# Optimization experiments

Hardware: AMD Instinct MI355X
Metric: run time of the kernel (lower is better)

Reference implementation:

```python
import jax, jax.numpy as jnp
import numpy as np

GRID = 32
N_NODES = GRID * GRID          # 1024
PATCH = 1
C_IN = 3
NODE_F = C_IN * PATCH * PATCH  # 3
HID = 256
N_CLASSES = 10


def _build_norm_adj():
    # 5-point grid stencil + self loops, symmetrically normalized: D^-1/2 A D^-1/2
    adj = np.zeros((N_NODES, N_NODES), dtype=np.float32)
    idx = np.arange(N_NODES)
    i, j = idx // GRID, idx % GRID
    adj[idx, idx] = 1.0
    for di, dj in [(-1, 0), (1, 0), (0, -1), (0, 1)]:
        ni, nj = i + di, j + dj
        ok = (ni >= 0) & (ni < GRID) & (nj >= 0) & (nj < GRID)
        adj[idx[ok], (ni * GRID + nj)[ok]] = 1.0
    deg = adj.sum(axis=1)
    dis = np.where(deg > 0, deg ** -0.5, 0.0).astype(np.float32)
    return jnp.asarray(dis[:, None] * adj * dis[None, :])


def _image_to_graph(x):
    # [B,C,H,W] -> [B, grid, patch, grid, patch] blocks -> [B, N, C*patch^2]
    B = x.shape[0]
    x = x.reshape(B, C_IN, GRID, PATCH, GRID, PATCH)
    x = jnp.transpose(x, (0, 2, 4, 1, 3, 5))
    return x.reshape(B, N_NODES, NODE_F)


def setup_inputs() -> dict:
    key = jax.random.key(0)
    ks = jax.random.split(key, 10)
    s = 0.05
    return {
        "x": jax.random.normal(ks[0], (256, 3, 32, 32), dtype=jnp.float32),
        "W1": jax.random.normal(ks[1], (HID, NODE_F), dtype=jnp.float32) * s,
        "b1": jnp.zeros((HID,), dtype=jnp.float32),
        "W2": jax.random.normal(ks[2], (HID, HID), dtype=jnp.float32) * s,
        "b2": jnp.zeros((HID,), dtype=jnp.float32),
        "W3": jax.random.normal(ks[3], (HID // 2, HID), dtype=jnp.float32) * s,
        "b3": jnp.zeros((HID // 2,), dtype=jnp.float32),
        "Wc": jax.random.normal(ks[4], (N_CLASSES, N_NODES * (HID // 2)), dtype=jnp.float32) * s,
        "bc": jnp.zeros((N_CLASSES,), dtype=jnp.float32),
        "adj": _build_norm_adj(),
    }


def _gc(h, W, b, adj):
    # Linear, then fixed-adjacency aggregation, then ReLU
    h = jnp.einsum('bnf,hf->bnh', h, W) + b
    h = jnp.einsum('mn,bnh->bmh', adj, h)
    return jax.nn.relu(h)


def reference(x, W1, b1, W2, b2, W3, b3, Wc, bc, adj):
    h = _image_to_graph(x)                 # [B, N, 3]
    h = _gc(h, W1, b1, adj)                # [B, N, 256]
    h = _gc(h, W2, b2, adj)                # [B, N, 256]
    h = _gc(h, W3, b3, adj)                # [B, N, 128]
    h = h.reshape(h.shape[0], -1)          # [B, N*128]
    return h @ Wc.T + bc                   # [B, 10]
```

## Files before the change

### kernel.cpp

```cpp
#include <hip/hip_runtime.h>
#include <stdint.h>

#define N_NODES 1024
#define NCLS 10
#define KDIM 131072

typedef unsigned short u16;
typedef __bf16 bf16x8 __attribute__((ext_vector_type(8)));
typedef float f32x4 __attribute__((ext_vector_type(4)));

__device__ __forceinline__ float b2f_lo(uint32_t u) {
  union { float f; uint32_t u; } v; v.u = u << 16; return v.f;
}
__device__ __forceinline__ float b2f_hi(uint32_t u) {
  union { float f; uint32_t u; } v; v.u = u & 0xFFFF0000u; return v.f;
}
__device__ __forceinline__ u16 f2b(float f) {
  union { float f; uint32_t u; } v; v.f = f;
  uint32_t r = v.u + 0x7FFF + ((v.u >> 16) & 1);
  return (u16)(r >> 16);
}
__device__ __forceinline__ uint32_t pkbf(float a, float b) {
#if __has_builtin(__builtin_amdgcn_cvt_pk_bf16_f32)
  typedef __bf16 bf2 __attribute__((ext_vector_type(2)));
  bf2 r = __builtin_amdgcn_cvt_pk_bf16_f32(a, b);
  union { bf2 v; uint32_t u; } c; c.v = r; return c.u;
#else
  union { float f; uint32_t u; } va, vb; va.f = a; vb.f = b;
  uint32_t ra = (va.u + 0x7FFF + ((va.u >> 16) & 1)) >> 16;
  uint32_t rb = (vb.u + 0x7FFF + ((vb.u >> 16) & 1)) & 0xFFFF0000u;
  return ra | rb;
#endif
}

__device__ __forceinline__ void async_copy16(const u16* g, u16* l) {
  __builtin_amdgcn_global_load_lds(
      (const __attribute__((address_space(1))) void*)g,
      (__attribute__((address_space(3))) void*)l, 16, 0, 0);
}

__device__ __forceinline__ void agg8(uint4 v, float c, float2* acc) {
  const uint32_t* u = (const uint32_t*)&v;
#pragma unroll
  for (int e = 0; e < 4; e++) {
    acc[e].x += c * b2f_lo(u[e]);
    acc[e].y += c * b2f_hi(u[e]);
  }
}

__global__ __launch_bounds__(256) void cvt_w_kernel(const float* __restrict__ w,
                                                    u16* __restrict__ o, int n) {
  int i = blockIdx.x * 256 + threadIdx.x;
  if (i < n) o[i] = f2b(w[i]);
}

__global__ __launch_bounds__(256) void prep_wc_kernel(const float* __restrict__ wc,
                                                      u16* __restrict__ o) {
  int i = blockIdx.x * 256 + threadIdx.x;
  int row = i >> 17;
  int col = i & (KDIM - 1);
  o[i] = (row < NCLS) ? f2b(wc[row * KDIM + col]) : (u16)0;
}

__global__ __launch_bounds__(256) void prep_tab_kernel(const float* __restrict__ adj,
                                                       int* __restrict__ nbi,
                                                       float* __restrict__ nbc,
                                                       float* __restrict__ r) {
  int m = blockIdx.x * 256 + threadIdx.x;
  if (m >= N_NODES) return;
  int i = m >> 5, j = m & 31;
  const float* arow = adj + (size_t)m * N_NODES;
  int n[5]; float c[5];
  n[0] = m;                      c[0] = arow[m];
  n[1] = (i > 0)  ? m - 32 : m;  c[1] = (i > 0)  ? arow[m - 32] : 0.f;
  n[2] = (i < 31) ? m + 32 : m;  c[2] = (i < 31) ? arow[m + 32] : 0.f;
  n[3] = (j > 0)  ? m - 1  : m;  c[3] = (j > 0)  ? arow[m - 1]  : 0.f;
  n[4] = (j < 31) ? m + 1  : m;  c[4] = (j < 31) ? arow[m + 1]  : 0.f;
  float s = 0.f;
#pragma unroll
  for (int t = 0; t < 5; t++) { nbi[m * 5 + t] = n[t]; nbc[m * 5 + t] = c[t]; s += c[t]; }
  r[m] = s;
}

__global__ __launch_bounds__(256) void outinit_kernel(const float* __restrict__ bc,
                                                      float* __restrict__ out) {
  int idx = blockIdx.x * 256 + threadIdx.x;
  if (idx < 256 * NCLS) out[idx] = bc[idx % NCLS];
}

__global__ __launch_bounds__(256) void l1agg_kernel(
    const float* __restrict__ x,
    const float* __restrict__ W1,
    const float* __restrict__ b1,
    const int* __restrict__ nbi, const float* __restrict__ nbc,
    const float* __restrict__ r,
    u16* __restrict__ g)
{
  __shared__ u16 h1s[128 * 256];
  __shared__ float gxs[128][4];
  __shared__ float W1s[768];
  __shared__ float b1s[256];
  int p0 = blockIdx.x * 64;
  int b = p0 >> 10;
  int m0 = p0 & 1023;
  int e0 = m0 - 32;
  int tid = threadIdx.x;

  b1s[tid] = b1[tid];
  for (int i = tid; i < 768; i += 256) W1s[i] = W1[i];

  if (tid < 128) {
    int n = e0 + tid;
    float g0 = 0.f, g1 = 0.f, g2 = 0.f, rn = 0.f;
    if (n >= 0 && n < N_NODES) {
      const float* xb = x + (size_t)b * 3072;
#pragma unroll
      for (int t = 0; t < 5; t++) {
        int nb = nbi[n * 5 + t]; float cf = nbc[n * 5 + t];
        g0 += cf * xb[nb];
        g1 += cf * xb[1024 + nb];
        g2 += cf * xb[2048 + nb];
      }
      rn = r[n];
    }
    gxs[tid][0] = g0; gxs[tid][1] = g1; gxs[tid][2] = g2; gxs[tid][3] = rn;
  }
  __syncthreads();

  int ch8 = (tid & 31) * 8;
  float w[8][3], bb[8];
#pragma unroll
  for (int c = 0; c < 8; c++) {
    w[c][0] = W1s[(ch8 + c) * 3];
    w[c][1] = W1s[(ch8 + c) * 3 + 1];
    w[c][2] = W1s[(ch8 + c) * 3 + 2];
    bb[c] = b1s[ch8 + c];
  }

#pragma unroll
  for (int it = 0; it < 16; it++) {
    int node = (tid >> 5) + it * 8;
    float g0 = gxs[node][0], g1 = gxs[node][1], g2 = gxs[node][2], rn = gxs[node][3];
    uint32_t pk[4];
#pragma unroll
    for (int c = 0; c < 8; c += 2) {
      float z0 = fmaxf(g0 * w[c][0] + g1 * w[c][1] + g2 * w[c][2] + rn * bb[c], 0.f);
      float z1 = fmaxf(g0 * w[c+1][0] + g1 * w[c+1][1] + g2 * w[c+1][2] + rn * bb[c+1], 0.f);
      pk[c >> 1] = pkbf(z0, z1);
    }
    *(uint4*)&h1s[node * 256 + ch8] = *(uint4*)pk;
  }
  __syncthreads();

#pragma unroll
  for (int it = 0; it < 8; it++) {
    int node = (tid >> 5) + it * 8;
    int m = m0 + node;
    float2 acc[4] = {};
#pragma unroll
    for (int t = 0; t < 5; t++) {
      int nb = nbi[m * 5 + t]; float cf = nbc[m * 5 + t];
      agg8(*(const uint4*)&h1s[(nb - e0) * 256 + ch8], cf, acc);
    }
    uint4 o;
    o.x = pkbf(acc[0].x, acc[0].y); o.y = pkbf(acc[1].x, acc[1].y);
    o.z = pkbf(acc[2].x, acc[2].y); o.w = pkbf(acc[3].x, acc[3].y);
    *(uint4*)&g[(size_t)(p0 + node) * 256 + ch8] = o;
  }
}

__global__ __launch_bounds__(256, 2) void mm_kernel(
    const u16* __restrict__ A, const u16* __restrict__ W,
    const float* __restrict__ bias, const float* __restrict__ r,
    u16* __restrict__ C, int N)
{
  const int K = 256;
  __shared__ u16 As[2][128 * 64];
  __shared__ u16 Bs[2][128 * 64];
  int n0 = blockIdx.x * 128;
  int m0 = blockIdx.y * 128;
  int tid = threadIdx.x;
  int w = tid >> 6, l = tid & 63;
  int wm = w >> 1, wn = w & 1;

  int r8 = l >> 3, oct = l & 7;
  int so = (oct ^ r8) << 3;
  const u16* ga0 = A + (size_t)(m0 + w * 32 + r8) * K + so;
  const u16* gb0 = W + (size_t)(n0 + w * 32 + r8) * K + so;

#define MM_ISSUE(kq, buf) \
  _Pragma("unroll") for (int q = 0; q < 4; q++) { \
    async_copy16(ga0 + (size_t)q * 8 * K + (kq) * 64, &As[buf][(w * 32 + q * 8) * 64]); \
    async_copy16(gb0 + (size_t)q * 8 * K + (kq) * 64, &Bs[buf][(w * 32 + q * 8) * 64]); \
  }

  MM_ISSUE(0, 0);

  f32x4 acc[4][4] = {};
  int lrow = l & 15, lq = l >> 4;
  int s = lrow & 7;

#pragma unroll
  for (int kq = 0; kq < 4; kq++) {
    int buf = kq & 1;
    __syncthreads();
    if (kq < 3) MM_ISSUE(kq + 1, buf ^ 1);
    const u16* pa = &As[buf][(wm * 64 + lrow) * 64];
    const u16* pb = &Bs[buf][(wn * 64 + lrow) * 64];
#pragma unroll
    for (int kh = 0; kh < 2; kh++) {
      int po = (((kh << 2) | lq) ^ s) << 3;
      bf16x8 af[4], bf[4];
#pragma unroll
      for (int t = 0; t < 4; t++) {
        af[t] = *(const bf16x8*)(pa + t * 16 * 64 + po);
        bf[t] = *(const bf16x8*)(pb + t * 16 * 64 + po);
      }
#pragma unroll
      for (int mt = 0; mt < 4; mt++)
#pragma unroll
        for (int nt = 0; nt < 4; nt++)
          acc[mt][nt] = __builtin_amdgcn_mfma_f32_16x16x32_bf16(af[mt], bf[nt], acc[mt][nt], 0, 0, 0);
    }
  }
#undef MM_ISSUE

#pragma unroll
  for (int mt = 0; mt < 4; mt++)
#pragma unroll
    for (int nt = 0; nt < 4; nt++) {
      f32x4 v = acc[mt][nt];
      int col = n0 + wn * 64 + nt * 16 + lrow;
      float bs = bias[col];
#pragma unroll
      for (int i2 = 0; i2 < 4; i2++) {
        int row = m0 + wm * 64 + mt * 16 + lq * 4 + i2;
        float val = v[i2] + r[row & 1023] * bs;
        C[(size_t)row * N + col] = f2b(fmaxf(val, 0.f));
      }
    }
}

__global__ __launch_bounds__(256, 2) void mm3agg_kernel(
    const u16* __restrict__ H,
    const u16* __restrict__ W,
    const float* __restrict__ bias, const float* __restrict__ r,
    const int* __restrict__ nbi, const float* __restrict__ nbc,
    u16* __restrict__ C)
{
  const int K = 256, N = 128;
  const int AST = 72;
  __shared__ u16 As[2][128 * AST];
  __shared__ u16 Bs[2][128 * 64];
  int m0 = blockIdx.x * 128;
  int tid = threadIdx.x;
  int w = tid >> 6, l = tid & 63;
  int wm = w >> 1, wn = w & 1;

  int arow = tid >> 1;
  int acol = (tid & 1) * 32;
  int pg = m0 + arow;
  int node = pg & 1023;
  const u16* hb = H + ((size_t)(pg >> 10) << 10) * 256 + acol;
  const u16* nbp[5]; float cf[5];
#pragma unroll
  for (int j = 0; j < 5; j++) {
    nbp[j] = hb + (size_t)nbi[node * 5 + j] * 256;
    cf[j] = nbc[node * 5 + j];
  }

  int r8 = l >> 3, oct = l & 7;
  int so = (oct ^ r8) << 3;
  const u16* gb0 = W + (size_t)(w * 32 + r8) * K + so;

#define M3_ISSUEB(kq, buf) \
  _Pragma("unroll") for (int q = 0; q < 4; q++) \
    async_copy16(gb0 + (size_t)q * 8 * K + (kq) * 64, &Bs[buf][(w * 32 + q * 8) * 64]);

#define M3_LOADA(kq) \
  _Pragma("unroll") for (int j = 0; j < 5; j++) \
    _Pragma("unroll") for (int q = 0; q < 4; q++) \
      L[j][q] = *(const uint4*)(nbp[j] + (kq) * 64 + q * 8);

#define M3_AGGSTORE(buf) { \
  u16* dst = &As[buf][arow * AST + acol]; \
  _Pragma("unroll") for (int q = 0; q < 4; q++) { \
    float2 acc2[4] = {}; \
    _Pragma("unroll") for (int j = 0; j < 5; j++) agg8(L[j][q], cf[j], acc2); \
    uint4 o; \
    o.x = pkbf(acc2[0].x, acc2[0].y); o.y = pkbf(acc2[1].x, acc2[1].y); \
    o.z = pkbf(acc2[2].x, acc2[2].y); o.w = pkbf(acc2[3].x, acc2[3].y); \
    *(uint4*)(dst + q * 8) = o; \
  } }

  uint4 L[5][4];
  M3_ISSUEB(0, 0);
  M3_LOADA(0);
  M3_AGGSTORE(0);

  f32x4 acc[4][4] = {};
  int lrow = l & 15, lq = l >> 4;
  int s = lrow & 7;

#pragma unroll
  for (int kq = 0; kq < 4; kq++) {
    int buf = kq & 1;
    __syncthreads();
    if (kq < 3) {
      M3_ISSUEB(kq + 1, buf ^ 1);
      M3_LOADA(kq + 1);
    }
    const u16* pa = &As[buf][(wm * 64 + lrow) * AST];
    const u16* pb = &Bs[buf][(wn * 64 + lrow) * 64];
#pragma unroll
    for (int kh = 0; kh < 2; kh++) {
      int po = (((kh << 2) | lq) ^ s) << 3;
      bf16x8 af[4], bf[4];
#pragma unroll
      for (int t = 0; t < 4; t++) {
        af[t] = *(const bf16x8*)(pa + t * 16 * AST + kh * 32 + lq * 8);
        bf[t] = *(const bf16x8*)(pb + t * 16 * 64 + po);
      }
#pragma unroll
      for (int mt = 0; mt < 4; mt++)
#pragma unroll
        for (int nt = 0; nt < 4; nt++)
          acc[mt][nt] = __builtin_amdgcn_mfma_f32_16x16x32_bf16(af[mt], bf[nt], acc[mt][nt], 0, 0, 0);
    }
    if (kq < 3) M3_AGGSTORE(buf ^ 1);
  }
#undef M3_ISSUEB
#undef M3_LOADA
#undef M3_AGGSTORE

#pragma unroll
  for (int mt = 0; mt < 4; mt++)
#pragma unroll
    for (int nt = 0; nt < 4; nt++) {
      f32x4 v = acc[mt][nt];
      int col = wn * 64 + nt * 16 + lrow;
      float bs = bias[col];
#pragma unroll
      for (int i2 = 0; i2 < 4; i2++) {
        int row = m0 + wm * 64 + mt * 16 + lq * 4 + i2;
        float val = v[i2] + r[row & 1023] * bs;
        C[(size_t)row * N + col] = f2b(fmaxf(val, 0.f));
      }
    }
}

__global__ __launch_bounds__(256) void cls_kernel(
    const u16* __restrict__ h3,
    const u16* __restrict__ Wcb,
    float* __restrict__ out,
    int b0)
{
  int mt = blockIdx.x;
  int split = blockIdx.y;
  int w = threadIdx.x >> 6, l = threadIdx.x & 63;
  int lrow = l & 15, lq = l >> 4;
  f32x4 acc = {};
  int kbase = split * 4096 + w * 1024;
  const u16* pa = h3 + (size_t)(mt * 16 + lrow) * KDIM + kbase + lq * 8;
  const u16* pb = Wcb + (size_t)lrow * KDIM + kbase + lq * 8;
#pragma unroll 4
  for (int kk = 0; kk < 1024; kk += 32) {
    bf16x8 a = *(const bf16x8*)(pa + kk);
    bf16x8 b = *(const bf16x8*)(pb + kk);
    acc = __builtin_amdgcn_mfma_f32_16x16x32_bf16(a, b, acc, 0, 0, 0);
  }
  if (lrow < NCLS) {
#pragma unroll
    for (int i2 = 0; i2 < 4; i2++) {
      int b = b0 + mt * 16 + lq * 4 + i2;
      atomicAdd(&out[b * NCLS + lrow], acc[i2]);
    }
  }
}

extern "C" void kernel_launch(void* const* d_in, const int* in_sizes, int n_in,
                              void* d_out, int out_size, void* d_ws, size_t ws_size,
                              hipStream_t stream) {
  const float* x   = (const float*)d_in[0];
  const float* W1  = (const float*)d_in[1];
  const float* b1  = (const float*)d_in[2];
  const float* W2  = (const float*)d_in[3];
  const float* b2  = (const float*)d_in[4];
  const float* W3  = (const float*)d_in[5];
  const float* b3  = (const float*)d_in[6];
  const float* Wc  = (const float*)d_in[7];
  const float* bc  = (const float*)d_in[8];
  const float* adj = (const float*)d_in[9];
  float* out = (float*)d_out;
  const int B = 256;

  uint8_t* ws = (uint8_t*)d_ws;
  u16* W2b = (u16*)ws;  ws += (size_t)256 * 256 * 2;
  u16* W3b = (u16*)ws;  ws += (size_t)128 * 256 * 2;
  u16* Wcb = (u16*)ws;  ws += (size_t)16 * KDIM * 2;
  float* rr  = (float*)ws; ws += 1024 * 4;
  int*   nbi = (int*)ws;   ws += 1024 * 5 * 4;
  float* nbc = (float*)ws; ws += 1024 * 5 * 4;
  uintptr_t al = ((uintptr_t)ws + 255) & ~(uintptr_t)255;
  ws = (uint8_t*)al;
  size_t used = (size_t)(ws - (uint8_t*)d_ws);
  size_t avail = (ws_size > used) ? ws_size - used : 0;
  int chunk = 256;
  while (chunk > 32 && (size_t)chunk * 1024 * 256 * 2 * 2 > avail) chunk >>= 1;
  u16* bufA = (u16*)ws;
  u16* bufB = bufA + (size_t)chunk * 1024 * 256;

  cvt_w_kernel<<<256, 256, 0, stream>>>(W2, W2b, 256 * 256);
  cvt_w_kernel<<<128, 256, 0, stream>>>(W3, W3b, 128 * 256);
  prep_wc_kernel<<<(16 * KDIM) / 256, 256, 0, stream>>>(Wc, Wcb);
  prep_tab_kernel<<<4, 256, 0, stream>>>(adj, nbi, nbc, rr);
  outinit_kernel<<<(256 * NCLS + 255) / 256, 256, 0, stream>>>(bc, out);

  for (int b0 = 0; b0 < B; b0 += chunk) {
    const float* xb = x + (size_t)b0 * 3 * 1024;
    int M = chunk * 1024;
    l1agg_kernel<<<M / 64, 256, 0, stream>>>(xb, W1, b1, nbi, nbc, rr, bufB);
    {
      dim3 g(2, M / 128);
      mm_kernel<<<g, 256, 0, stream>>>(bufB, W2b, b2, rr, bufA, 256);
    }
    mm3agg_kernel<<<M / 128, 256, 0, stream>>>(bufA, W3b, b3, rr, nbi, nbc, bufB);
    dim3 gc(chunk / 16, 32);
    cls_kernel<<<gc, 256, 0, stream>>>(bufB, Wcb, out, b0);
  }
}
```

Before: 349.6 us.

## Halve GEMM K-tile to 32, raise occupancy, and use packed f32x2 math

Both GEMM kernels (mm_kernel and the fused aggregate+GEMM mm3agg_kernel) now stage 32-wide K slices instead of 64, with 8 pipeline steps instead of 4. This shrinks LDS use and register pressure, so launch bounds rise to 4 and 3 blocks per SM. The XOR swizzle on B tiles is dropped in favour of a plain 32-column layout, which may add LDS bank conflicts. Aggregation and layer-1 elementwise math are rewritten with f32x2 vectors to encourage packed FMA instructions. More barriers per tile are the trade-off.

```diff
diff --git a/kernel.cpp b/kernel.cpp
--- a/kernel.cpp
+++ b/kernel.cpp
@@ -8,6 +8,7 @@
 typedef unsigned short u16;
 typedef __bf16 bf16x8 __attribute__((ext_vector_type(8)));
 typedef float f32x4 __attribute__((ext_vector_type(4)));
+typedef float f32x2 __attribute__((ext_vector_type(2)));
 
 __device__ __forceinline__ float b2f_lo(uint32_t u) {
   union { float f; uint32_t u; } v; v.u = u << 16; return v.f;
@@ -32,6 +33,7 @@
   return ra | rb;
 #endif
 }
+__device__ __forceinline__ uint32_t pkbf2(f32x2 z) { return pkbf(z.x, z.y); }
 
 __device__ __forceinline__ void async_copy16(const u16* g, u16* l) {
   __builtin_amdgcn_global_load_lds(
@@ -39,12 +41,13 @@
       (__attribute__((address_space(3))) void*)l, 16, 0, 0);
 }
 
-__device__ __forceinline__ void agg8(uint4 v, float c, float2* acc) {
+__device__ __forceinline__ void agg8p(uint4 v, float c, f32x2* acc) {
   const uint32_t* u = (const uint32_t*)&v;
+  f32x2 cv = {c, c};
 #pragma unroll
   for (int e = 0; e < 4; e++) {
-    acc[e].x += c * b2f_lo(u[e]);
-    acc[e].y += c * b2f_hi(u[e]);
+    f32x2 p = {b2f_lo(u[e]), b2f_hi(u[e])};
+    acc[e] += p * cv;
   }
 }
 
@@ -128,25 +131,29 @@
   __syncthreads();
 
   int ch8 = (tid & 31) * 8;
-  float w[8][3], bb[8];
-#pragma unroll
-  for (int c = 0; c < 8; c++) {
-    w[c][0] = W1s[(ch8 + c) * 3];
-    w[c][1] = W1s[(ch8 + c) * 3 + 1];
-    w[c][2] = W1s[(ch8 + c) * 3 + 2];
-    bb[c] = b1s[ch8 + c];
+  f32x2 wp[3][4], bp[4];
+#pragma unroll
+  for (int p = 0; p < 4; p++) {
+    int c = ch8 + 2 * p;
+    wp[0][p] = (f32x2){W1s[c * 3],     W1s[(c + 1) * 3]};
+    wp[1][p] = (f32x2){W1s[c * 3 + 1], W1s[(c + 1) * 3 + 1]};
+    wp[2][p] = (f32x2){W1s[c * 3 + 2], W1s[(c + 1) * 3 + 2]};
+    bp[p]    = (f32x2){b1s[c],         b1s[c + 1]};
   }
 
 #pragma unroll
   for (int it = 0; it < 16; it++) {
     int node = (tid >> 5) + it * 8;
-    float g0 = gxs[node][0], g1 = gxs[node][1], g2 = gxs[node][2], rn = gxs[node][3];
+    f32x2 g0v = {gxs[node][0], gxs[node][0]};
+    f32x2 g1v = {gxs[node][1], gxs[node][1]};
+    f32x2 g2v = {gxs[node][2], gxs[node][2]};
+    f32x2 rnv = {gxs[node][3], gxs[node][3]};
     uint32_t pk[4];
 #pragma unroll
-    for (int c = 0; c < 8; c += 2) {
-      float z0 = fmaxf(g0 * w[c][0] + g1 * w[c][1] + g2 * w[c][2] + rn * bb[c], 0.f);
-      float z1 = fmaxf(g0 * w[c+1][0] + g1 * w[c+1][1] + g2 * w[c+1][2] + rn * bb[c+1], 0.f);
-      pk[c >> 1] = pkbf(z0, z1);
+    for (int p = 0; p < 4; p++) {
+      f32x2 z = g0v * wp[0][p] + g1v * wp[1][p] + g2v * wp[2][p] + rnv * bp[p];
+      z.x = fmaxf(z.x, 0.f); z.y = fmaxf(z.y, 0.f);
+      pk[p] = pkbf2(z);
     }
     *(uint4*)&h1s[node * 256 + ch8] = *(uint4*)pk;
   }
@@ -156,72 +163,67 @@
   for (int it = 0; it < 8; it++) {
     int node = (tid >> 5) + it * 8;
     int m = m0 + node;
-    float2 acc[4] = {};
+    f32x2 acc[4] = {};
 #pragma unroll
     for (int t = 0; t < 5; t++) {
       int nb = nbi[m * 5 + t]; float cf = nbc[m * 5 + t];
-      agg8(*(const uint4*)&h1s[(nb - e0) * 256 + ch8], cf, acc);
+      agg8p(*(const uint4*)&h1s[(nb - e0) * 256 + ch8], cf, acc);
     }
     uint4 o;
-    o.x = pkbf(acc[0].x, acc[0].y); o.y = pkbf(acc[1].x, acc[1].y);
-    o.z = pkbf(acc[2].x, acc[2].y); o.w = pkbf(acc[3].x, acc[3].y);
+    o.x = pkbf2(acc[0]); o.y = pkbf2(acc[1]);
+    o.z = pkbf2(acc[2]); o.w = pkbf2(acc[3]);
     *(uint4*)&g[(size_t)(p0 + node) * 256 + ch8] = o;
   }
 }
 
-__global__ __launch_bounds__(256, 2) void mm_kernel(
+__global__ __launch_bounds__(256, 4) void mm_kernel(
     const u16* __restrict__ A, const u16* __restrict__ W,
     const float* __restrict__ bias, const float* __restrict__ r,
     u16* __restrict__ C, int N)
 {
   const int K = 256;
-  __shared__ u16 As[2][128 * 64];
-  __shared__ u16 Bs[2][128 * 64];
+  __shared__ u16 As[2][128 * 32];
+  __shared__ u16 Bs[2][128 * 32];
   int n0 = blockIdx.x * 128;
   int m0 = blockIdx.y * 128;
   int tid = threadIdx.x;
   int w = tid >> 6, l = tid & 63;
   int wm = w >> 1, wn = w & 1;
 
-  int r8 = l >> 3, oct = l & 7;
-  int so = (oct ^ r8) << 3;
-  const u16* ga0 = A + (size_t)(m0 + w * 32 + r8) * K + so;
-  const u16* gb0 = W + (size_t)(n0 + w * 32 + r8) * K + so;
+  int srow = w * 16 + (l >> 2);
+  int skoff = (l & 3) * 8;
+  const u16* ga0 = A + (size_t)(m0 + srow) * K + skoff;
+  const u16* gb0 = W + (size_t)(n0 + srow) * K + skoff;
 
 #define MM_ISSUE(kq, buf) \
-  _Pragma("unroll") for (int q = 0; q < 4; q++) { \
-    async_copy16(ga0 + (size_t)q * 8 * K + (kq) * 64, &As[buf][(w * 32 + q * 8) * 64]); \
-    async_copy16(gb0 + (size_t)q * 8 * K + (kq) * 64, &Bs[buf][(w * 32 + q * 8) * 64]); \
+  _Pragma("unroll") for (int q = 0; q < 2; q++) { \
+    async_copy16(ga0 + (size_t)q * 64 * K + (kq) * 32, &As[buf][(q * 64 + w * 16) * 32]); \
+    async_copy16(gb0 + (size_t)q * 64 * K + (kq) * 32, &Bs[buf][(q * 64 + w * 16) * 32]); \
   }
 
   MM_ISSUE(0, 0);
 
   f32x4 acc[4][4] = {};
   int lrow = l & 15, lq = l >> 4;
-  int s = lrow & 7;
-
-#pragma unroll
-  for (int kq = 0; kq < 4; kq++) {
+
+#pragma unroll
+  for (int kq = 0; kq < 8; kq++) {
     int buf = kq & 1;
     __syncthreads();
-    if (kq < 3) MM_ISSUE(kq + 1, buf ^ 1);
-    const u16* pa = &As[buf][(wm * 64 + lrow) * 64];
-    const u16* pb = &Bs[buf][(wn * 64 + lrow) * 64];
-#pragma unroll
-    for (int kh = 0; kh < 2; kh++) {
-      int po = (((kh << 2) | lq) ^ s) << 3;
-      bf16x8 af[4], bf[4];
-#pragma unroll
-      for (int t = 0; t < 4; t++) {
-        af[t] = *(const bf16x8*)(pa + t * 16 * 64 + po);
-        bf[t] = *(const bf16x8*)(pb + t * 16 * 64 + po);
-      }
-#pragma unroll
-      for (int mt = 0; mt < 4; mt++)
-#pragma unroll
-        for (int nt = 0; nt < 4; nt++)
-          acc[mt][nt] = __builtin_amdgcn_mfma_f32_16x16x32_bf16(af[mt], bf[nt], acc[mt][nt], 0, 0, 0);
-    }
+    if (kq < 7) MM_ISSUE(kq + 1, buf ^ 1);
+    const u16* pa = &As[buf][(wm * 64 + lrow) * 32 + lq * 8];
+    const u16* pb = &Bs[buf][(wn * 64 + lrow) * 32 + lq * 8];
+    bf16x8 af[4], bf[4];
+#pragma unroll
+    for (int t = 0; t < 4; t++) {
+      af[t] = *(const bf16x8*)(pa + t * 16 * 32);
+      bf[t] = *(const bf16x8*)(pb + t * 16 * 32);
+    }
+#pragma unroll
+    for (int mt = 0; mt < 4; mt++)
+#pragma unroll
+      for (int nt = 0; nt < 4; nt++)
+        acc[mt][nt] = __builtin_amdgcn_mfma_f32_16x16x32_bf16(af[mt], bf[nt], acc[mt][nt], 0, 0, 0);
   }
 #undef MM_ISSUE
 
@@ -241,7 +243,7 @@
     }
 }
 
-__global__ __launch_bounds__(256, 2) void mm3agg_kernel(
+__global__ __launch_bounds__(256, 3) void mm3agg_kernel(
     const u16* __restrict__ H,
     const u16* __restrict__ W,
     const float* __restrict__ bias, const float* __restrict__ r,
@@ -249,16 +251,16 @@
     u16* __restrict__ C)
 {
   const int K = 256, N = 128;
-  const int AST = 72;
+  const int AST = 40;
   __shared__ u16 As[2][128 * AST];
-  __shared__ u16 Bs[2][128 * 64];
+  __shared__ u16 Bs[2][128 * 32];
   int m0 = blockIdx.x * 128;
   int tid = threadIdx.x;
   int w = tid >> 6, l = tid & 63;
   int wm = w >> 1, wn = w & 1;
 
   int arow = tid >> 1;
-  int acol = (tid & 1) * 32;
+  int acol = (tid & 1) * 16;
   int pg = m0 + arow;
   int node = pg & 1023;
   const u16* hb = H + ((size_t)(pg >> 10) << 10) * 256 + acol;
@@ -269,65 +271,60 @@
     cf[j] = nbc[node * 5 + j];
   }
 
-  int r8 = l >> 3, oct = l & 7;
-  int so = (oct ^ r8) << 3;
-  const u16* gb0 = W + (size_t)(w * 32 + r8) * K + so;
+  int srow = w * 16 + (l >> 2);
+  int skoff = (l & 3) * 8;
+  const u16* gb0 = W + (size_t)srow * K + skoff;
 
 #define M3_ISSUEB(kq, buf) \
-  _Pragma("unroll") for (int q = 0; q < 4; q++) \
-    async_copy16(gb0 + (size_t)q * 8 * K + (kq) * 64, &Bs[buf][(w * 32 + q * 8) * 64]);
+  _Pragma("unroll") for (int q = 0; q < 2; q++) \
+    async_copy16(gb0 + (size_t)q * 64 * K + (kq) * 32, &Bs[buf][(q * 64 + w * 16) * 32]);
 
 #define M3_LOADA(kq) \
   _Pragma("unroll") for (int j = 0; j < 5; j++) \
-    _Pragma("unroll") for (int q = 0; q < 4; q++) \
-      L[j][q] = *(const uint4*)(nbp[j] + (kq) * 64 + q * 8);
+    _Pragma("unroll") for (int q = 0; q < 2; q++) \
+      L[j][q] = *(const uint4*)(nbp[j] + (kq) * 32 + q * 8);
 
 #define M3_AGGSTORE(buf) { \
   u16* dst = &As[buf][arow * AST + acol]; \
-  _Pragma("unroll") for (int q = 0; q < 4; q++) { \
-    float2 acc2[4] = {}; \
-    _Pragma("unroll") for (int j = 0; j < 5; j++) agg8(L[j][q], cf[j], acc2); \
+  _Pragma("unroll") for (int q = 0; q < 2; q++) { \
+    f32x2 a2[4] = {}; \
+    _Pragma("unroll") for (int j = 0; j < 5; j++) agg8p(L[j][q], cf[j], a2); \
     uint4 o; \
-    o.x = pkbf(acc2[0].x, acc2[0].y); o.y = pkbf(acc2[1].x, acc2[1].y); \
-    o.z = pkbf(acc2[2].x, acc2[2].y); o.w = pkbf(acc2[3].x, acc2[3].y); \
+    o.x = pkbf2(a2[0]); o.y = pkbf2(a2[1]); \
+    o.z = pkbf2(a2[2]); o.w = pkbf2(a2[3]); \
     *(uint4*)(dst + q * 8) = o; \
   } }
 
-  uint4 L[5][4];
+  uint4 L[5][2];
   M3_ISSUEB(0, 0);
   M3_LOADA(0);
   M3_AGGSTORE(0);
 
   f32x4 acc[4][4] = {};
   int lrow = l & 15, lq = l >> 4;
-  int s = lrow & 7;
-
-#pragma unroll
-  for (int kq = 0; kq < 4; kq++) {
+
+#pragma unroll
+  for (int kq = 0; kq < 8; kq++) {
     int buf = kq & 1;
     __syncthreads();
-    if (kq < 3) {
+    if (kq < 7) {
       M3_ISSUEB(kq + 1, buf ^ 1);
       M3_LOADA(kq + 1);
     }
-    const u16* pa = &As[buf][(wm * 64 + lrow) * AST];
-    const u16* pb = &Bs[buf][(wn * 64 + lrow) * 64];
-#pragma unroll
-    for (int kh = 0; kh < 2; kh++) {
-      int po = (((kh << 2) | lq) ^ s) << 3;
-      bf16x8 af[4], bf[4];
-#pragma unroll
-      for (int t = 0; t < 4; t++) {
-        af[t] = *(const bf16x8*)(pa + t * 16 * AST + kh * 32 + lq * 8);
-        bf[t] = *(const bf16x8*)(pb + t * 16 * 64 + po);
-      }
-#pragma unroll
-      for (int mt = 0; mt < 4; mt++)
-#pragma unroll
-        for (int nt = 0; nt < 4; nt++)
-          acc[mt][nt] = __builtin_amdgcn_mfma_f32_16x16x32_bf16(af[mt], bf[nt], acc[mt][nt], 0, 0, 0);
-    }
-    if (kq < 3) M3_AGGSTORE(buf ^ 1);
+    const u16* pa = &As[buf][(wm * 64 + lrow) * AST + lq * 8];
+    const u16* pb = &Bs[buf][(wn * 64 + lrow) * 32 + lq * 8];
+    bf16x8 af[4], bf[4];
+#pragma unroll
+    for (int t = 0; t < 4; t++) {
+      af[t] = *(const bf16x8*)(pa + t * 16 * AST);
+      bf[t] = *(const bf16x8*)(pb + t * 16 * 32);
+    }
+#pragma unroll
+    for (int mt = 0; mt < 4; mt++)
+#pragma unroll
+      for (int nt = 0; nt < 4; nt++)
+        acc[mt][nt] = __builtin_amdgcn_mfma_f32_16x16x32_bf16(af[mt], bf[nt], acc[mt][nt], 0, 0, 0);
+    if (kq < 7) M3_AGGSTORE(buf ^ 1);
   }
 #undef M3_ISSUEB
 #undef M3_LOADA
```

After: 379.7 us. 1.09x slower.
